# Optimization experiments

Hardware: AMD Instinct MI355X
Metric: run time of the kernel (lower is better)

## Reference

```python
import jax, jax.numpy as jnp
import numpy as np

B, S, D, H = 2, 2048, 2048, 16  # batch, seq, d_model, n_heads
LN_EPS = 1e-6  # flax nn.LayerNorm default


def _layernorm(x, scale):
    mu = jnp.mean(x, axis=-1, keepdims=True)
    var = jnp.var(x, axis=-1, keepdims=True)
    return (x - mu) * jax.lax.rsqrt(var + LN_EPS) * scale


def setup_inputs() -> dict:
    key = jax.random.key(0)
    ks = jax.random.split(key, 5)
    x = jax.random.normal(ks[0], (B, S, D), dtype=jnp.float32)
    # ALiBi-style bias, broadcastable over batch and query positions
    attn_bias = jax.random.normal(ks[1], (1, H, 1, S), dtype=jnp.float32)
    attention_mask = jnp.ones((B, S), dtype=jnp.int32)
    w_qkv = jax.random.normal(ks[2], (D, 3 * D), dtype=jnp.float32) * 0.01
    b_qkv = jnp.zeros((3 * D,), dtype=jnp.float32)
    wo = jax.random.normal(ks[3], (D, D), dtype=jnp.float32) * 0.01
    b_wo = jnp.zeros((D,), dtype=jnp.float32)
    q_ln_scale = jnp.ones((D,), dtype=jnp.float32)
    k_ln_scale = jnp.ones((D,), dtype=jnp.float32)
    return {"x": x, "attn_bias": attn_bias, "attention_mask": attention_mask,
            "w_qkv": w_qkv, "b_qkv": b_qkv, "wo": wo, "b_wo": b_wo,
            "q_ln_scale": q_ln_scale, "k_ln_scale": k_ln_scale}


def reference(x, attn_bias, attention_mask, w_qkv, b_qkv, wo, b_wo, q_ln_scale, k_ln_scale):
    b, s, ds = x.shape
    h = H
    d = ds // h  # head dim
    qkv = jnp.einsum('bsd,df->bsf', x, w_qkv) + b_qkv
    q, k, v = jnp.split(qkv, 3, axis=-1)
    # qk-LayerNorm is over the FULL d_model, before head split (as in source)
    q = _layernorm(q, q_ln_scale)
    k = _layernorm(k, k_ln_scale)
    q = q.reshape(b, s, h, d)
    k = k.reshape(b, s, h, d)
    v = v.reshape(b, s, h, d)
    atw = jnp.einsum('bqhd,bkhd->bhqk', q, k) * jax.lax.rsqrt(jnp.asarray(d, v.dtype))
    atw = atw + attn_bias  # ALiBi bias
    mv = jnp.finfo(atw.dtype).min
    # causal mask [1,1,s,s]
    causal = jnp.tril(jnp.ones((s, s), dtype=bool))[None, None]
    # padding mask: 0 where attended, min where masked
    pad = jnp.where(attention_mask.reshape(b, 1, 1, s) == 1, 0.0, mv).astype(atw.dtype)
    atw = atw + pad
    atw = atw + jnp.where(causal, 0.0, mv).astype(atw.dtype)
    atw = jax.nn.softmax(atw, axis=-1)
    out = jnp.einsum('bhqk,bkhd->bqhd', atw, v).reshape(b, s, ds)
    return jnp.einsum('bsd,de->bse', out, wo) + b_wo
```

## Files before the change

kernel.cpp:

```cpp
#include <hip/hip_runtime.h>
#include <stdint.h>
#include <stddef.h>


typedef __attribute__((ext_vector_type(8))) short bf16x8;
typedef __attribute__((ext_vector_type(4))) float f32x4;

#define MFMA16(a, b, c) __builtin_amdgcn_mfma_f32_16x16x32_bf16((a), (b), (c), 0, 0, 0)

__device__ __forceinline__ void async_copy16(void* lds, const void* g) {
  __builtin_amdgcn_global_load_lds(
      (const __attribute__((address_space(1))) void*)g,
      (__attribute__((address_space(3))) void*)lds, 16, 0, 0);
}

__device__ __forceinline__ short f2bf(float f) {
  union { float f; uint32_t u; } v; v.f = f;
  uint32_t r = (v.u + 0x7fffu + ((v.u >> 16) & 1u)) >> 16;
  return (short)(uint16_t)r;
}

__device__ __forceinline__ float bf2f(short s) {
  union { float f; uint32_t u; } v;
  v.u = ((uint32_t)(uint16_t)s) << 16;
  return v.f;
}

#define ATT_SCALE 0.08838834764831845f
#define VMDRAIN asm volatile("s_waitcnt vmcnt(0)" ::: "memory")

__global__ __launch_bounds__(256) void cvt_f32_bf16(const float* __restrict__ in,
                                                    short* __restrict__ out) {
  size_t i = ((size_t)blockIdx.x * 256 + threadIdx.x) * 8;
  f32x4 a = *(const f32x4*)(in + i);
  f32x4 b = *(const f32x4*)(in + i + 4);
  bf16x8 o;
#pragma unroll
  for (int j = 0; j < 4; ++j) { o[j] = f2bf(a[j]); o[4 + j] = f2bf(b[j]); }
  *(bf16x8*)(out + i) = o;
}

__global__ __launch_bounds__(256) void transpose_cvt(const float* __restrict__ in,
                                                     short* __restrict__ out,
                                                     int R, int C) {
  __shared__ float t[64][65];
  const int tid = threadIdx.x;
  const int c0 = blockIdx.x * 64, r0 = blockIdx.y * 64;
#pragma unroll
  for (int i = 0; i < 16; ++i) {
    int idx = i * 256 + tid;
    int r = idx >> 6, c = idx & 63;
    t[r][c] = in[(size_t)(r0 + r) * C + c0 + c];
  }
  __syncthreads();
#pragma unroll
  for (int i = 0; i < 16; ++i) {
    int idx = i * 256 + tid;
    int cc = idx >> 6, rr = idx & 63;
    out[(size_t)(c0 + cc) * R + r0 + rr] = f2bf(t[rr][cc]);
  }
}

__global__ __launch_bounds__(256) void transpose_v_bf(const short* __restrict__ qkv,
                                                      short* __restrict__ vt) {
  __shared__ short t[64][65];
  const int tid = threadIdx.x;
  const int d0 = blockIdx.x * 64;
  const int s0 = blockIdx.y * 64;
  const int bh = blockIdx.z;
  const int b = bh >> 4, h = bh & 15;
#pragma unroll
  for (int i = 0; i < 16; ++i) {
    int idx = i * 256 + tid;
    int r = idx >> 6, c = idx & 63;
    t[r][c] = qkv[(size_t)(b * 2048 + s0 + r) * 6144 + 4096 + h * 128 + d0 + c];
  }
  __syncthreads();
#pragma unroll
  for (int i = 0; i < 16; ++i) {
    int idx = i * 256 + tid;
    int dd = idx >> 6, ss = idx & 63;
    vt[((size_t)(bh * 128 + d0 + dd)) * 2048 + s0 + ss] = t[ss][dd];
  }
}

__global__ __launch_bounds__(256) void ln_qk(const short* __restrict__ qkv,
                                             const float* __restrict__ qsc,
                                             const float* __restrict__ ksc,
                                             short* __restrict__ q_bf,
                                             short* __restrict__ k_bf) {
  __shared__ float redS[2][4], redQ[2][4];
  const int row = blockIdx.x, tid = threadIdx.x;
  const int lane = tid & 63, wave = tid >> 6;
  const short* base = qkv + (size_t)row * 6144;
#pragma unroll
  for (int part = 0; part < 2; ++part) {
    const short* p = base + part * 2048 + tid * 8;
    bf16x8 v8 = *(const bf16x8*)p;
    float f[8];
#pragma unroll
    for (int j = 0; j < 8; ++j) f[j] = bf2f(v8[j]);
    float s = 0.f, sq = 0.f;
#pragma unroll
    for (int j = 0; j < 8; ++j) { s += f[j]; sq += f[j] * f[j]; }
#pragma unroll
    for (int d = 1; d < 64; d <<= 1) { s += __shfl_xor(s, d); sq += __shfl_xor(sq, d); }
    if (lane == 0) { redS[part][wave] = s; redQ[part][wave] = sq; }
    __syncthreads();
    float tot  = redS[part][0] + redS[part][1] + redS[part][2] + redS[part][3];
    float totq = redQ[part][0] + redQ[part][1] + redQ[part][2] + redQ[part][3];
    float mean = tot * (1.f / 2048.f);
    float var  = totq * (1.f / 2048.f) - mean * mean;
    float rstd = rsqrtf(var + 1e-6f) * (part == 0 ? ATT_SCALE : 1.0f);
    const float* scp = (part == 0 ? qsc : ksc) + tid * 8;
    f32x4 s0 = *(const f32x4*)scp;
    f32x4 s1 = *(const f32x4*)(scp + 4);
    bf16x8 o;
#pragma unroll
    for (int j = 0; j < 4; ++j) {
      o[j]     = f2bf((f[j] - mean) * rstd * s0[j]);
      o[4 + j] = f2bf((f[4 + j] - mean) * rstd * s1[j]);
    }
    short* outp = (part == 0 ? q_bf : k_bf) + (size_t)row * 2048 + tid * 8;
    *(bf16x8*)outp = o;
  }
}

template <typename OutT>
__global__ __launch_bounds__(256, 2) void gemm_bt_bias(const short* __restrict__ A,
                                                       const short* __restrict__ BT,
                                                       const float* __restrict__ bias,
                                                       OutT* __restrict__ C,
                                                       int M, int N, int K) {
  __shared__ alignas(16) short a_lds[128 * 32];
  __shared__ alignas(16) short b_lds[128 * 32];
  const int tid = threadIdx.x;
  const int lane = tid & 63, wave = tid >> 6;
  const int wr = wave >> 1, wc = wave & 1;
  const int tn = blockIdx.x, tm = blockIdx.y;
  const int r15 = lane & 15, hi = lane >> 4;

  const short* Ab = A + (size_t)tm * 128 * K;
  const short* Bb = BT + (size_t)tn * 128 * K;

  f32x4 acc[4][4];
  const f32x4 Z = {0.f, 0.f, 0.f, 0.f};
#pragma unroll
  for (int m = 0; m < 4; ++m)
#pragma unroll
    for (int n = 0; n < 4; ++n) acc[m][n] = Z;

  for (int k0 = 0; k0 < K; k0 += 32) {
    __syncthreads();
#pragma unroll
    for (int j = 0; j < 2; ++j) {
      int c = j * 256 + tid;
      int row = c >> 2, col = (c & 3) << 3;
      async_copy16(&a_lds[c << 3], Ab + (size_t)row * K + k0 + col);
      async_copy16(&b_lds[c << 3], Bb + (size_t)row * K + k0 + col);
    }
    __syncthreads();
    bf16x8 af[4], bfr[4];
#pragma unroll
    for (int m = 0; m < 4; ++m)
      af[m] = *(const bf16x8*)&a_lds[(wr * 64 + m * 16 + r15) * 32 + hi * 8];
#pragma unroll
    for (int n = 0; n < 4; ++n)
      bfr[n] = *(const bf16x8*)&b_lds[(wc * 64 + n * 16 + r15) * 32 + hi * 8];
#pragma unroll
    for (int m = 0; m < 4; ++m)
#pragma unroll
      for (int n = 0; n < 4; ++n) acc[m][n] = MFMA16(af[m], bfr[n], acc[m][n]);
  }

  const int r0 = tm * 128 + wr * 64;
  const int c0 = tn * 128 + wc * 64;
#pragma unroll
  for (int n = 0; n < 4; ++n) {
    float bv = bias[c0 + n * 16 + r15];
#pragma unroll
    for (int m = 0; m < 4; ++m) {
#pragma unroll
      for (int r = 0; r < 4; ++r) {
        float val = acc[m][n][r] + bv;
        size_t idx = (size_t)(r0 + m * 16 + hi * 4 + r) * N + c0 + n * 16 + r15;
        if constexpr (sizeof(OutT) == 2) C[idx] = (OutT)f2bf(val);
        else                             C[idx] = val;
      }
    }
  }
}

__global__ __launch_bounds__(256) void attn_fwd(const short* __restrict__ q_bf,
                                                const short* __restrict__ k_bf,
                                                const short* __restrict__ vt,
                                                const float* __restrict__ abias,
                                                const int* __restrict__ amask,
                                                short* __restrict__ out_bf) {
  __shared__ alignas(16) short K_lds[64 * 128];
  __shared__ alignas(16) short V_lds[128 * 64];
  __shared__ alignas(16) short p_lds[4][16 * 64];
  __shared__ float bias_c[2048];

  const int tid = threadIdx.x, lane = tid & 63, wave = tid >> 6;
  const int qt = 31 - blockIdx.x;
  const int h = blockIdx.y, b = blockIdx.z;
  const int r15 = lane & 15, hi = lane >> 4;

  for (int i = tid; i < 2048; i += 256) {
    float bb = abias[h * 2048 + i];
    if (amask[b * 2048 + i] == 0) bb = -1e30f;
    bias_c[i] = bb;
  }

  const int qrow = b * 2048 + qt * 64 + wave * 16 + r15;
  bf16x8 qf[4];
#pragma unroll
  for (int kb = 0; kb < 4; ++kb)
    qf[kb] = *(const bf16x8*)(q_bf + (size_t)qrow * 2048 + h * 128 + kb * 32 + hi * 8);

  f32x4 O[8];
  const f32x4 Z = {0.f, 0.f, 0.f, 0.f};
#pragma unroll
  for (int n = 0; n < 8; ++n) O[n] = Z;
  f32x4 Ol = Z;
  float m_run[4];
#pragma unroll
  for (int r = 0; r < 4; ++r) m_run[r] = -3e38f;

  const short one_bf = (short)0x3F80;
  const bf16x8 ones_f = {one_bf, one_bf, one_bf, one_bf,
                         one_bf, one_bf, one_bf, one_bf};
  const int qg0 = qt * 64 + wave * 16 + hi * 4;
  const int ntiles = qt + 1;

  for (int kt = 0; kt < ntiles; ++kt) {
    __syncthreads();

#pragma unroll
    for (int j = 0; j < 4; ++j) {
      int c = j * 256 + tid;
      int kr = c >> 4, kc = (c & 15) ^ (kr & 7);
      async_copy16(&K_lds[c << 3],
                   k_bf + (size_t)(b * 2048 + kt * 64 + kr) * 2048 + h * 128 + (kc << 3));
      int vr = c >> 3, vc = (c & 7) ^ (vr & 7);
      async_copy16(&V_lds[c << 3],
                   vt + ((size_t)((b * 16 + h) * 128 + vr)) * 2048 + kt * 64 + (vc << 3));
    }
    VMDRAIN;
    __syncthreads();

    f32x4 s[4];
#pragma unroll
    for (int ks = 0; ks < 4; ++ks) {
      s[ks] = Z;
#pragma unroll
      for (int kb = 0; kb < 4; ++kb) {
        int row = ks * 16 + r15;
        int ch = (kb * 4 + hi) ^ (row & 7);
        bf16x8 kf = *(const bf16x8*)&K_lds[row * 128 + ch * 8];
        s[ks] = MFMA16(qf[kb], kf, s[ks]);
      }
    }

    if (kt == qt) {
#pragma unroll
      for (int ks = 0; ks < 4; ++ks) {
        int kg = kt * 64 + ks * 16 + r15;
        float bb = bias_c[kg];
#pragma unroll
        for (int r = 0; r < 4; ++r) {
          float v = s[ks][r] + bb;
          if (kg > qg0 + r) v = -1e30f;
          s[ks][r] = v;
        }
      }
    } else {
#pragma unroll
      for (int ks = 0; ks < 4; ++ks) {
        float bb = bias_c[kt * 64 + ks * 16 + r15];
#pragma unroll
        for (int r = 0; r < 4; ++r) s[ks][r] += bb;
      }
    }

    float corr[4];
#pragma unroll
    for (int r = 0; r < 4; ++r) {
      float mx = fmaxf(fmaxf(s[0][r], s[1][r]), fmaxf(s[2][r], s[3][r]));
      mx = fmaxf(mx, __shfl_xor(mx, 1));
      mx = fmaxf(mx, __shfl_xor(mx, 2));
      mx = fmaxf(mx, __shfl_xor(mx, 4));
      mx = fmaxf(mx, __shfl_xor(mx, 8));
      float mn = fmaxf(m_run[r], mx);
      corr[r] = __expf(m_run[r] - mn);
      m_run[r] = mn;
#pragma unroll
      for (int ks = 0; ks < 4; ++ks) s[ks][r] = __expf(s[ks][r] - mn);
    }
#pragma unroll
    for (int r = 0; r < 4; ++r) {
      Ol[r] *= corr[r];
#pragma unroll
      for (int n = 0; n < 8; ++n) O[n][r] *= corr[r];
    }

    short* pw = &p_lds[wave][0];
#pragma unroll
    for (int r = 0; r < 4; ++r) {
      int q = hi * 4 + r;
      int qs = (q & 7) << 3;
      uint32_t pk0, pk1;
      asm("v_cvt_pk_bf16_f32 %0, %1, %2" : "=v"(pk0) : "v"(s[0][r]), "v"(s[1][r]));
      asm("v_cvt_pk_bf16_f32 %0, %1, %2" : "=v"(pk1) : "v"(s[2][r]), "v"(s[3][r]));
      pw[q * 64 + ((r15) ^ qs)]      = (short)pk0;
      pw[q * 64 + ((16 + r15) ^ qs)] = (short)(pk0 >> 16);
      pw[q * 64 + ((32 + r15) ^ qs)] = (short)pk1;
      pw[q * 64 + ((48 + r15) ^ qs)] = (short)(pk1 >> 16);
    }

    bf16x8 pf[2];
#pragma unroll
    for (int kb = 0; kb < 2; ++kb)
      pf[kb] = *(const bf16x8*)&pw[r15 * 64 + ((kb * 32 + hi * 8) ^ ((r15 & 7) << 3))];

#pragma unroll
    for (int n = 0; n < 8; ++n) {
#pragma unroll
      for (int kb = 0; kb < 2; ++kb) {
        int row = n * 16 + r15;
        int ch = (kb * 4 + hi) ^ (row & 7);
        bf16x8 vf = *(const bf16x8*)&V_lds[row * 64 + ch * 8];
        O[n] = MFMA16(pf[kb], vf, O[n]);
      }
    }
    Ol = MFMA16(pf[0], ones_f, Ol);
    Ol = MFMA16(pf[1], ones_f, Ol);
  }

  float inv[4];
#pragma unroll
  for (int r = 0; r < 4; ++r) inv[r] = 1.0f / Ol[r];
  const int orow = b * 2048 + qt * 64 + wave * 16;
#pragma unroll
  for (int n = 0; n < 8; ++n)
#pragma unroll
    for (int r = 0; r < 4; ++r)
      out_bf[(size_t)(orow + hi * 4 + r) * 2048 + h * 128 + n * 16 + r15] =
          f2bf(O[n][r] * inv[r]);
}

extern "C" void kernel_launch(void* const* d_in, const int* in_sizes, int n_in,
                              void* d_out, int out_size, void* d_ws, size_t ws_size,
                              hipStream_t stream) {
  const float* x     = (const float*)d_in[0];
  const float* abias = (const float*)d_in[1];
  const int*   amask = (const int*)d_in[2];
  const float* w_qkv = (const float*)d_in[3];
  const float* b_qkv = (const float*)d_in[4];
  const float* wo    = (const float*)d_in[5];
  const float* b_wo  = (const float*)d_in[6];
  const float* q_ln  = (const float*)d_in[7];
  const float* k_ln  = (const float*)d_in[8];
  float* out = (float*)d_out;

  char* ws = (char*)d_ws;
  short* x_bf   = (short*)(ws);
  short* wqkvT  = (short*)(ws + 16777216);
  short* woT    = (short*)(ws + 41943040);
  short* q_bf   = (short*)(ws + 50331648);
  short* k_bf   = (short*)(ws + 67108864);
  short* vt     = (short*)(ws + 83886080);
  short* out_bf = (short*)(ws + 100663296);
  short* qkv_bf = (short*)(ws + 117440512);

  cvt_f32_bf16<<<4096, 256, 0, stream>>>(x, x_bf);
  transpose_cvt<<<dim3(96, 32), 256, 0, stream>>>(w_qkv, wqkvT, 2048, 6144);
  transpose_cvt<<<dim3(32, 32), 256, 0, stream>>>(wo, woT, 2048, 2048);
  gemm_bt_bias<short><<<dim3(48, 32), 256, 0, stream>>>(x_bf, wqkvT, b_qkv, qkv_bf,
                                                        4096, 6144, 2048);
  ln_qk<<<4096, 256, 0, stream>>>(qkv_bf, q_ln, k_ln, q_bf, k_bf);
  transpose_v_bf<<<dim3(2, 32, 32), 256, 0, stream>>>(qkv_bf, vt);
  attn_fwd<<<dim3(32, 16, 2), 256, 0, stream>>>(q_bf, k_bf, vt, abias, amask, out_bf);
  gemm_bt_bias<float><<<dim3(16, 32), 256, 0, stream>>>(out_bf, woT, b_wo, out,
                                                        4096, 2048, 2048);
}
```

Before: 378.2 us.

## Process two 64-row query groups per attention block to reuse K/V tiles

```diff
diff --git a/kernel.cpp b/kernel.cpp
--- a/kernel.cpp
+++ b/kernel.cpp
@@ -199,11 +199,11 @@
                                                 short* __restrict__ out_bf) {
   __shared__ alignas(16) short K_lds[64 * 128];
   __shared__ alignas(16) short V_lds[128 * 64];
-  __shared__ alignas(16) short p_lds[4][16 * 64];
+  __shared__ alignas(16) short p_lds[4][32 * 64];
   __shared__ float bias_c[2048];
 
   const int tid = threadIdx.x, lane = tid & 63, wave = tid >> 6;
-  const int qt = 31 - blockIdx.x;
+  const int qt = 15 - blockIdx.x;
   const int h = blockIdx.y, b = blockIdx.z;
   const int r15 = lane & 15, hi = lane >> 4;
 
@@ -213,26 +213,33 @@
     bias_c[i] = bb;
   }
 
-  const int qrow = b * 2048 + qt * 64 + wave * 16 + r15;
-  bf16x8 qf[4];
-#pragma unroll
-  for (int kb = 0; kb < 4; ++kb)
-    qf[kb] = *(const bf16x8*)(q_bf + (size_t)qrow * 2048 + h * 128 + kb * 32 + hi * 8);
-
-  f32x4 O[8];
+  bf16x8 qf[2][4];
+#pragma unroll
+  for (int g = 0; g < 2; ++g) {
+    const int qrow = b * 2048 + qt * 128 + g * 64 + wave * 16 + r15;
+#pragma unroll
+    for (int kb = 0; kb < 4; ++kb)
+      qf[g][kb] =
+          *(const bf16x8*)(q_bf + (size_t)qrow * 2048 + h * 128 + kb * 32 + hi * 8);
+  }
+
+  f32x4 O[2][8];
   const f32x4 Z = {0.f, 0.f, 0.f, 0.f};
 #pragma unroll
-  for (int n = 0; n < 8; ++n) O[n] = Z;
-  f32x4 Ol = Z;
-  float m_run[4];
-#pragma unroll
-  for (int r = 0; r < 4; ++r) m_run[r] = -3e38f;
+  for (int g = 0; g < 2; ++g)
+#pragma unroll
+    for (int n = 0; n < 8; ++n) O[g][n] = Z;
+  f32x4 Ol[2] = {Z, Z};
+  float m_run[2][4];
+#pragma unroll
+  for (int g = 0; g < 2; ++g)
+#pragma unroll
+    for (int r = 0; r < 4; ++r) m_run[g][r] = -3e38f;
 
   const short one_bf = (short)0x3F80;
   const bf16x8 ones_f = {one_bf, one_bf, one_bf, one_bf,
                          one_bf, one_bf, one_bf, one_bf};
-  const int qg0 = qt * 64 + wave * 16 + hi * 4;
-  const int ntiles = qt + 1;
+  const int ntiles = 2 * qt + 2;
 
   for (int kt = 0; kt < ntiles; ++kt) {
     __syncthreads();
@@ -250,104 +257,118 @@
     VMDRAIN;
     __syncthreads();
 
-    f32x4 s[4];
-#pragma unroll
-    for (int ks = 0; ks < 4; ++ks) {
-      s[ks] = Z;
-#pragma unroll
-      for (int kb = 0; kb < 4; ++kb) {
-        int row = ks * 16 + r15;
-        int ch = (kb * 4 + hi) ^ (row & 7);
-        bf16x8 kf = *(const bf16x8*)&K_lds[row * 128 + ch * 8];
-        s[ks] = MFMA16(qf[kb], kf, s[ks]);
-      }
+#pragma unroll
+    for (int g = 0; g < 2; ++g) {
+      if (kt > 2 * qt + g) continue;
+
+      f32x4 s[4];
+      __builtin_amdgcn_s_setprio(1);
+#pragma unroll
+      for (int ks = 0; ks < 4; ++ks) {
+        s[ks] = Z;
+#pragma unroll
+        for (int kb = 0; kb < 4; ++kb) {
+          int row = ks * 16 + r15;
+          int ch = (kb * 4 + hi) ^ (row & 7);
+          bf16x8 kf = *(const bf16x8*)&K_lds[row * 128 + ch * 8];
+          s[ks] = MFMA16(qf[g][kb], kf, s[ks]);
+        }
+      }
+      __builtin_amdgcn_s_setprio(0);
+
+      if (kt >= 2 * qt + g) {
+        const int qg0 = qt * 128 + g * 64 + wave * 16 + hi * 4;
+#pragma unroll
+        for (int ks = 0; ks < 4; ++ks) {
+          int kg = kt * 64 + ks * 16 + r15;
+          float bb = bias_c[kg];
+#pragma unroll
+          for (int r = 0; r < 4; ++r) {
+            float v = s[ks][r] + bb;
+            if (kg > qg0 + r) v = -1e30f;
+            s[ks][r] = v;
+          }
+        }
+      } else {
+#pragma unroll
+        for (int ks = 0; ks < 4; ++ks) {
+          float bb = bias_c[kt * 64 + ks * 16 + r15];
+#pragma unroll
+          for (int r = 0; r < 4; ++r) s[ks][r] += bb;
+        }
+      }
+
+      float corr[4];
+#pragma unroll
+      for (int r = 0; r < 4; ++r) {
+        float mx = fmaxf(fmaxf(s[0][r], s[1][r]), fmaxf(s[2][r], s[3][r]));
+        mx = fmaxf(mx, __shfl_xor(mx, 1));
+        mx = fmaxf(mx, __shfl_xor(mx, 2));
+        mx = fmaxf(mx, __shfl_xor(mx, 4));
+        mx = fmaxf(mx, __shfl_xor(mx, 8));
+        float mn = fmaxf(m_run[g][r], mx);
+        corr[r] = __expf(m_run[g][r] - mn);
+        m_run[g][r] = mn;
+#pragma unroll
+        for (int ks = 0; ks < 4; ++ks) s[ks][r] = __expf(s[ks][r] - mn);
+      }
+#pragma unroll
+      for (int r = 0; r < 4; ++r) {
+        Ol[g][r] *= corr[r];
+#pragma unroll
+        for (int n = 0; n < 8; ++n) O[g][n][r] *= corr[r];
+      }
+
+      short* pw = &p_lds[wave][0];
+#pragma unroll
+      for (int r = 0; r < 4; ++r) {
+        int q = g * 16 + hi * 4 + r;
+        int qs = (q & 7) << 3;
+        uint32_t pk0, pk1;
+        asm("v_cvt_pk_bf16_f32 %0, %1, %2" : "=v"(pk0) : "v"(s[0][r]), "v"(s[1][r]));
+        asm("v_cvt_pk_bf16_f32 %0, %1, %2" : "=v"(pk1) : "v"(s[2][r]), "v"(s[3][r]));
+        pw[q * 64 + ((r15) ^ qs)]      = (short)pk0;
+        pw[q * 64 + ((16 + r15) ^ qs)] = (short)(pk0 >> 16);
+        pw[q * 64 + ((32 + r15) ^ qs)] = (short)pk1;
+        pw[q * 64 + ((48 + r15) ^ qs)] = (short)(pk1 >> 16);
+      }
+
+      bf16x8 pf[2];
+#pragma unroll
+      for (int kb = 0; kb < 2; ++kb)
+        pf[kb] = *(const bf16x8*)&pw[(g * 16 + r15) * 64 +
+                                     ((kb * 32 + hi * 8) ^ ((r15 & 7) << 3))];
+
+      __builtin_amdgcn_s_setprio(1);
+#pragma unroll
+      for (int n = 0; n < 8; ++n) {
+#pragma unroll
+        for (int kb = 0; kb < 2; ++kb) {
+          int row = n * 16 + r15;
+          int ch = (kb * 4 + hi) ^ (row & 7);
+          bf16x8 vf = *(const bf16x8*)&V_lds[row * 64 + ch * 8];
+          O[g][n] = MFMA16(pf[kb], vf, O[g][n]);
+        }
+      }
+      Ol[g] = MFMA16(pf[0], ones_f, Ol[g]);
+      Ol[g] = MFMA16(pf[1], ones_f, Ol[g]);
+      __builtin_amdgcn_s_setprio(0);
     }
-
-    if (kt == qt) {
-#pragma unroll
-      for (int ks = 0; ks < 4; ++ks) {
-        int kg = kt * 64 + ks * 16 + r15;
-        float bb = bias_c[kg];
-#pragma unroll
-        for (int r = 0; r < 4; ++r) {
-          float v = s[ks][r] + bb;
-          if (kg > qg0 + r) v = -1e30f;
-          s[ks][r] = v;
-        }
-      }
-    } else {
-#pragma unroll
-      for (int ks = 0; ks < 4; ++ks) {
-        float bb = bias_c[kt * 64 + ks * 16 + r15];
-#pragma unroll
-        for (int r = 0; r < 4; ++r) s[ks][r] += bb;
-      }
-    }
-
-    float corr[4];
-#pragma unroll
-    for (int r = 0; r < 4; ++r) {
-      float mx = fmaxf(fmaxf(s[0][r], s[1][r]), fmaxf(s[2][r], s[3][r]));
-      mx = fmaxf(mx, __shfl_xor(mx, 1));
-      mx = fmaxf(mx, __shfl_xor(mx, 2));
-      mx = fmaxf(mx, __shfl_xor(mx, 4));
-      mx = fmaxf(mx, __shfl_xor(mx, 8));
-      float mn = fmaxf(m_run[r], mx);
-      corr[r] = __expf(m_run[r] - mn);
-      m_run[r] = mn;
-#pragma unroll
-      for (int ks = 0; ks < 4; ++ks) s[ks][r] = __expf(s[ks][r] - mn);
-    }
-#pragma unroll
-    for (int r = 0; r < 4; ++r) {
-      Ol[r] *= corr[r];
-#pragma unroll
-      for (int n = 0; n < 8; ++n) O[n][r] *= corr[r];
-    }
-
-    short* pw = &p_lds[wave][0];
-#pragma unroll
-    for (int r = 0; r < 4; ++r) {
-      int q = hi * 4 + r;
-      int qs = (q & 7) << 3;
-      uint32_t pk0, pk1;
-      asm("v_cvt_pk_bf16_f32 %0, %1, %2" : "=v"(pk0) : "v"(s[0][r]), "v"(s[1][r]));
-      asm("v_cvt_pk_bf16_f32 %0, %1, %2" : "=v"(pk1) : "v"(s[2][r]), "v"(s[3][r]));
-      pw[q * 64 + ((r15) ^ qs)]      = (short)pk0;
-      pw[q * 64 + ((16 + r15) ^ qs)] = (short)(pk0 >> 16);
-      pw[q * 64 + ((32 + r15) ^ qs)] = (short)pk1;
-      pw[q * 64 + ((48 + r15) ^ qs)] = (short)(pk1 >> 16);
-    }
-
-    bf16x8 pf[2];
-#pragma unroll
-    for (int kb = 0; kb < 2; ++kb)
-      pf[kb] = *(const bf16x8*)&pw[r15 * 64 + ((kb * 32 + hi * 8) ^ ((r15 & 7) << 3))];
-
-#pragma unroll
-    for (int n = 0; n < 8; ++n) {
-#pragma unroll
-      for (int kb = 0; kb < 2; ++kb) {
-        int row = n * 16 + r15;
-        int ch = (kb * 4 + hi) ^ (row & 7);
-        bf16x8 vf = *(const bf16x8*)&V_lds[row * 64 + ch * 8];
-        O[n] = MFMA16(pf[kb], vf, O[n]);
-      }
-    }
-    Ol = MFMA16(pf[0], ones_f, Ol);
-    Ol = MFMA16(pf[1], ones_f, Ol);
-  }
-
-  float inv[4];
-#pragma unroll
-  for (int r = 0; r < 4; ++r) inv[r] = 1.0f / Ol[r];
-  const int orow = b * 2048 + qt * 64 + wave * 16;
-#pragma unroll
-  for (int n = 0; n < 8; ++n)
-#pragma unroll
-    for (int r = 0; r < 4; ++r)
-      out_bf[(size_t)(orow + hi * 4 + r) * 2048 + h * 128 + n * 16 + r15] =
-          f2bf(O[n][r] * inv[r]);
+  }
+
+#pragma unroll
+  for (int g = 0; g < 2; ++g) {
+    float inv[4];
+#pragma unroll
+    for (int r = 0; r < 4; ++r) inv[r] = 1.0f / Ol[g][r];
+    const int orow = b * 2048 + qt * 128 + g * 64 + wave * 16;
+#pragma unroll
+    for (int n = 0; n < 8; ++n)
+#pragma unroll
+      for (int r = 0; r < 4; ++r)
+        out_bf[(size_t)(orow + hi * 4 + r) * 2048 + h * 128 + n * 16 + r15] =
+            f2bf(O[g][n][r] * inv[r]);
+  }
 }
 
 extern "C" void kernel_launch(void* const* d_in, const int* in_sizes, int n_in,
@@ -381,7 +402,7 @@
                                                         4096, 6144, 2048);
   ln_qk<<<4096, 256, 0, stream>>>(qkv_bf, q_ln, k_ln, q_bf, k_bf);
   transpose_v_bf<<<dim3(2, 32, 32), 256, 0, stream>>>(qkv_bf, vt);
-  attn_fwd<<<dim3(32, 16, 2), 256, 0, stream>>>(q_bf, k_bf, vt, abias, amask, out_bf);
+  attn_fwd<<<dim3(16, 16, 2), 256, 0, stream>>>(q_bf, k_bf, vt, abias, amask, out_bf);
   gemm_bt_bias<float><<<dim3(16, 32), 256, 0, stream>>>(out_bf, woT, b_wo, out,
                                                         4096, 2048, 2048);
 }
```

Measured after the change: 454.5 us. 1.2x slower.
